# Performance work log

Measured on AMD Instinct MI355X. Metric: run time of the kernel, lower is better.

The kernel has to match this reference:

```python
import jax, jax.numpy as jnp
import numpy as np

N_NODES, N_EDGES = 100000, 1600000
F_IN, F_OUT = 256, 64
N_REL, N_BASES = 2, 30


def setup_inputs() -> dict:
    key = jax.random.key(0)
    ks = jax.random.split(key, 6)
    x = jax.random.normal(ks[0], (N_NODES, F_IN), jnp.float32)
    edge_index = jax.random.randint(ks[1], (2, N_EDGES), 0, N_NODES, jnp.int32)
    edge_type = jax.random.randint(ks[2], (N_EDGES,), 0, N_REL, jnp.int32)
    basis = jax.random.normal(ks[3], (N_BASES, F_IN, F_OUT), jnp.float32) * 0.05
    att = jax.random.normal(ks[4], (N_REL, N_BASES), jnp.float32) * 0.2
    root = jax.random.normal(ks[5], (F_IN, F_OUT), jnp.float32) * 0.05
    bias = jnp.zeros((F_OUT,), jnp.float32)
    return dict(x=x, edge_index=edge_index, edge_type=edge_type,
                basis=basis, att=att, root=root, bias=bias)


def reference(x, edge_index, edge_type, basis, att, root, bias):
    # RGCN with basis decomposition (PyG RGCNConv, aggr='mean', edge_norm=None)
    n = x.shape[0]
    # relation weights from bases: [R, F_in, F_out]
    w = jnp.einsum('rb,bio->rio', att, basis)
    # transform all nodes under every relation once (R is tiny): [R, N, F_out]
    h = jnp.einsum('ni,rio->rno', x, w)
    src, dst = edge_index[0], edge_index[1]
    # per-edge message x_src @ W[edge_type]: gather [E, F_out]
    msg = h[edge_type, src]
    # mean aggregation over incoming edges at each target node
    agg = jax.ops.segment_sum(msg, dst, num_segments=n)
    cnt = jax.ops.segment_sum(jnp.ones((msg.shape[0],), x.dtype), dst, num_segments=n)
    agg = agg / jnp.maximum(cnt, 1.0)[:, None]
    # update: self-loop (root) transform + bias
    return agg + x @ root + bias
```

## Files before the change

### kernel.cpp

```cpp
#include <hip/hip_runtime.h>
#include <hip/hip_bf16.h>

#define N_NODES 100000
#define N_EDGES 1600000
#define F_IN    256
#define F_OUT   64
#define N_REL   2
#define N_BASES 30
#define SCAN_BS 512
#define N_SBLK  ((N_NODES + SCAN_BS - 1) / SCAN_BS)
#define N_NT    12
#define N_KS    8

typedef __attribute__((ext_vector_type(8))) short bf16x8;
typedef __attribute__((ext_vector_type(4))) float f32x4;

__device__ inline unsigned short f2bf(float f) {
    unsigned u = __float_as_uint(f);
    unsigned r = u + 0x7FFF + ((u >> 16) & 1);
    return (unsigned short)(r >> 16);
}
__device__ inline float bf2f(unsigned short b) {
    return __uint_as_float(((unsigned)b) << 16);
}

__global__ __launch_bounds__(256) void wcomp_kernel(
    const float* __restrict__ att, const float* __restrict__ basis,
    const float* __restrict__ root,
    unsigned short* __restrict__ wb_hi, unsigned short* __restrict__ wb_lo)
{
    int idx = blockIdx.x * 256 + threadIdx.x;
    if (idx >= N_KS * N_NT * 64) return;
    const int lane  = idx & 63;
    const int nt    = (idx >> 6) % N_NT;
    const int ks    = idx / (N_NT * 64);
    const int c     = nt * 16 + (lane & 15);
    const int kbase = ks * 32 + (lane >> 4) * 8;
    const int m     = c >> 6;
    const int f     = c & 63;

    bf16x8 hi, lo;
    #pragma unroll
    for (int i = 0; i < 8; ++i) {
        int k = kbase + i;
        float v;
        if (m == 2) {
            v = root[k * F_OUT + f];
        } else {
            v = 0.f;
            #pragma unroll
            for (int b = 0; b < N_BASES; ++b)
                v += att[m * N_BASES + b] * basis[((long)b * F_IN + k) * F_OUT + f];
        }
        unsigned short h = f2bf(v);
        unsigned short l = f2bf(v - bf2f(h));
        hi[i] = (short)h;
        lo[i] = (short)l;
    }
    *reinterpret_cast<bf16x8*>(wb_hi + (long)idx * 8) = hi;
    *reinterpret_cast<bf16x8*>(wb_lo + (long)idx * 8) = lo;
}

__global__ __launch_bounds__(256) void gemm_kernel(
    const float* __restrict__ x,
    const unsigned short* __restrict__ wb_hi,
    const unsigned short* __restrict__ wb_lo,
    const float* __restrict__ bias,
    float* __restrict__ h, float* __restrict__ out)
{
    const int lane = threadIdx.x & 63;
    const int wv   = threadIdx.x >> 6;
    const long row0 = (long)blockIdx.x * 128 + wv * 32;
    if (row0 >= N_NODES) return;

    const int mrow = lane & 15;
    const int kgrp = lane >> 4;

    f32x4 acc[2][N_NT];
    #pragma unroll
    for (int mt = 0; mt < 2; ++mt)
        #pragma unroll
        for (int nt = 0; nt < N_NT; ++nt)
            acc[mt][nt] = (f32x4){0.f, 0.f, 0.f, 0.f};

    const float* xp = x + (row0 + mrow) * F_IN + kgrp * 8;

    for (int ks = 0; ks < N_KS; ++ks) {
        bf16x8 ah[2], al[2];
        #pragma unroll
        for (int mt = 0; mt < 2; ++mt) {
            const float* p = xp + (long)mt * 16 * F_IN + ks * 32;
            float4 f0 = *reinterpret_cast<const float4*>(p);
            float4 f1 = *reinterpret_cast<const float4*>(p + 4);
            float fv[8] = {f0.x, f0.y, f0.z, f0.w, f1.x, f1.y, f1.z, f1.w};
            #pragma unroll
            for (int i = 0; i < 8; ++i) {
                unsigned short hb = f2bf(fv[i]);
                ah[mt][i] = (short)hb;
                al[mt][i] = (short)f2bf(fv[i] - bf2f(hb));
            }
        }
        const unsigned short* bh_base = wb_hi + ((long)(ks * N_NT) * 64 + lane) * 8;
        const unsigned short* bl_base = wb_lo + ((long)(ks * N_NT) * 64 + lane) * 8;
        #pragma unroll
        for (int nt = 0; nt < N_NT; ++nt) {
            bf16x8 bh = *reinterpret_cast<const bf16x8*>(bh_base + (long)nt * 64 * 8);
            bf16x8 bl = *reinterpret_cast<const bf16x8*>(bl_base + (long)nt * 64 * 8);
            #pragma unroll
            for (int mt = 0; mt < 2; ++mt) {
                acc[mt][nt] = __builtin_amdgcn_mfma_f32_16x16x32_bf16(ah[mt], bh, acc[mt][nt], 0, 0, 0);
                acc[mt][nt] = __builtin_amdgcn_mfma_f32_16x16x32_bf16(al[mt], bh, acc[mt][nt], 0, 0, 0);
                acc[mt][nt] = __builtin_amdgcn_mfma_f32_16x16x32_bf16(ah[mt], bl, acc[mt][nt], 0, 0, 0);
            }
        }
    }

    const int ccol = lane & 15;
    const int rsub = (lane >> 4) * 4;
    #pragma unroll
    for (int mt = 0; mt < 2; ++mt) {
        #pragma unroll
        for (int nt = 0; nt < N_NT; ++nt) {
            const int rel = nt >> 2;
            const int fc  = (nt & 3) * 16 + ccol;
            float badd = (rel == 2) ? bias[fc] : 0.f;
            #pragma unroll
            for (int i = 0; i < 4; ++i) {
                long row = row0 + mt * 16 + rsub + i;
                float v = acc[mt][nt][i] + badd;
                if (rel == 2) out[row * F_OUT + fc] = v;
                else          h[((long)rel * N_NODES + row) * F_OUT + fc] = v;
            }
        }
    }
}

__global__ __launch_bounds__(256) void hist_kernel(
    const int* __restrict__ edge_index, int* __restrict__ hist)
{
    int e = blockIdx.x * 256 + threadIdx.x;
    if (e >= N_EDGES) return;
    atomicAdd(&hist[edge_index[N_EDGES + e]], 1);
}

__global__ __launch_bounds__(SCAN_BS) void scanA_kernel(
    const int* __restrict__ hist, int* __restrict__ offs, int* __restrict__ bsum)
{
    __shared__ int s[SCAN_BS];
    const int t = threadIdx.x;
    const int i = blockIdx.x * SCAN_BS + t;
    int v = (i < N_NODES) ? hist[i] : 0;
    s[t] = v;
    __syncthreads();
    #pragma unroll
    for (int off = 1; off < SCAN_BS; off <<= 1) {
        int y = (t >= off) ? s[t - off] : 0;
        __syncthreads();
        if (t >= off) s[t] += y;
        __syncthreads();
    }
    if (i < N_NODES) offs[i] = s[t] - v;
    if (t == SCAN_BS - 1) bsum[blockIdx.x] = s[t];
}

__global__ __launch_bounds__(256) void scanB_kernel(
    const int* __restrict__ bsum, int* __restrict__ bpre)
{
    __shared__ int s[256];
    const int t = threadIdx.x;
    int v = (t < N_SBLK) ? bsum[t] : 0;
    s[t] = v;
    __syncthreads();
    #pragma unroll
    for (int off = 1; off < 256; off <<= 1) {
        int y = (t >= off) ? s[t - off] : 0;
        __syncthreads();
        if (t >= off) s[t] += y;
        __syncthreads();
    }
    if (t < N_SBLK) bpre[t] = s[t] - v;
}

__global__ __launch_bounds__(256) void pass2_kernel(
    const int* __restrict__ edge_index, const int* __restrict__ edge_type,
    const int* __restrict__ offs, const int* __restrict__ bpre,
    int* __restrict__ cur, int* __restrict__ elist)
{
    int e = blockIdx.x * 256 + threadIdx.x;
    if (e >= N_EDGES) return;
    int src = edge_index[e];
    int dst = edge_index[N_EDGES + e];
    int et  = edge_type[e];
    int pos = offs[dst] + bpre[dst >> 9] + atomicAdd(&cur[dst], 1);
    elist[pos] = src | (et << 20);
}

__global__ __launch_bounds__(256) void gather_kernel(
    const int* __restrict__ hist, const int* __restrict__ offs,
    const int* __restrict__ bpre, const int* __restrict__ elist,
    const float* __restrict__ h, float* __restrict__ out)
{
    const int lane = threadIdx.x & 63;
    const int nid  = blockIdx.x * 4 + (threadIdx.x >> 6);
    if (nid >= N_NODES) return;
    const int cnt  = hist[nid];
    const int base = offs[nid] + bpre[nid >> 9];

    float acc = 0.f;
    int j = 0;
    for (; j + 4 <= cnt; j += 4) {
        int e0 = elist[base + j];
        int e1 = elist[base + j + 1];
        int e2 = elist[base + j + 2];
        int e3 = elist[base + j + 3];
        float v0 = h[((long)(e0 >> 20) * N_NODES + (e0 & 0xFFFFF)) * F_OUT + lane];
        float v1 = h[((long)(e1 >> 20) * N_NODES + (e1 & 0xFFFFF)) * F_OUT + lane];
        float v2 = h[((long)(e2 >> 20) * N_NODES + (e2 & 0xFFFFF)) * F_OUT + lane];
        float v3 = h[((long)(e3 >> 20) * N_NODES + (e3 & 0xFFFFF)) * F_OUT + lane];
        acc += v0; acc += v1; acc += v2; acc += v3;
    }
    for (; j < cnt; ++j) {
        int e = elist[base + j];
        acc += h[((long)(e >> 20) * N_NODES + (e & 0xFFFFF)) * F_OUT + lane];
    }
    float inv = 1.0f / fmaxf((float)cnt, 1.0f);
    out[(long)nid * F_OUT + lane] += acc * inv;
}

extern "C" void kernel_launch(void* const* d_in, const int* in_sizes, int n_in,
                              void* d_out, int out_size, void* d_ws, size_t ws_size,
                              hipStream_t stream)
{
    const float* x          = (const float*)d_in[0];
    const int*   edge_index = (const int*)  d_in[1];
    const int*   edge_type  = (const int*)  d_in[2];
    const float* basis      = (const float*)d_in[3];
    const float* att        = (const float*)d_in[4];
    const float* root       = (const float*)d_in[5];
    const float* bias       = (const float*)d_in[6];
    float* out = (float*)d_out;

    char* ws = (char*)d_ws;
    size_t off = 0;
    unsigned short* wb_hi = (unsigned short*)(ws + off); off += (size_t)N_KS * N_NT * 64 * 8 * 2;
    unsigned short* wb_lo = (unsigned short*)(ws + off); off += (size_t)N_KS * N_NT * 64 * 8 * 2;
    float* h     = (float*)(ws + off); off += (size_t)N_REL * N_NODES * F_OUT * 4;
    int*   hist  = (int*)  (ws + off); off += (size_t)N_NODES * 4;
    int*   cur   = (int*)  (ws + off); off += (size_t)N_NODES * 4;
    int*   offs  = (int*)  (ws + off); off += (size_t)N_NODES * 4;
    int*   bsum  = (int*)  (ws + off); off += (size_t)N_SBLK * 4;
    int*   bpre  = (int*)  (ws + off); off += (size_t)N_SBLK * 4;
    int*   elist = (int*)  (ws + off); off += (size_t)N_EDGES * 4;

    hipMemsetAsync(hist, 0, (size_t)2 * N_NODES * 4, stream);

    wcomp_kernel<<<(N_KS * N_NT * 64 + 255) / 256, 256, 0, stream>>>(
        att, basis, root, wb_hi, wb_lo);

    gemm_kernel<<<(N_NODES + 127) / 128, 256, 0, stream>>>(
        x, wb_hi, wb_lo, bias, h, out);

    hist_kernel<<<(N_EDGES + 255) / 256, 256, 0, stream>>>(edge_index, hist);

    scanA_kernel<<<N_SBLK, SCAN_BS, 0, stream>>>(hist, offs, bsum);

    scanB_kernel<<<1, 256, 0, stream>>>(bsum, bpre);

    pass2_kernel<<<(N_EDGES + 255) / 256, 256, 0, stream>>>(
        edge_index, edge_type, offs, bpre, cur, elist);

    gather_kernel<<<(N_NODES + 3) / 4, 256, 0, stream>>>(
        hist, offs, bpre, elist, h, out);
}
```

Baseline: 466.7 us.

## Replace per-node atomic CSR scatter with two-level bucket scatter plus local sort

Edges are first scattered into 128-node buckets using padded per-bucket atomic counters. A second kernel then places each bucket's edges into per-node CSR order using shared-memory atomics. This replaces 1.6M global atomics spread over 100K random counters, and the scattered writes that go with them, with fewer contended counters and more localized writes. The cost is an extra pass over the edge list and two extra launches. The gather loop is also unrolled to 8 edges so more loads are in flight at once.

```diff
diff --git a/kernel.cpp b/kernel.cpp
--- a/kernel.cpp
+++ b/kernel.cpp
@@ -11,6 +11,7 @@
 #define N_SBLK  ((N_NODES + SCAN_BS - 1) / SCAN_BS)
 #define N_NT    12
 #define N_KS    8
+#define NB      ((N_NODES + 127) / 128)
 
 typedef __attribute__((ext_vector_type(8))) short bf16x8;
 typedef __attribute__((ext_vector_type(4))) float f32x4;
@@ -181,18 +182,55 @@
     if (t < N_SBLK) bpre[t] = s[t] - v;
 }
 
-__global__ __launch_bounds__(256) void pass2_kernel(
+__global__ __launch_bounds__(256) void bbase_kernel(
+    const int* __restrict__ offs, const int* __restrict__ bpre,
+    int* __restrict__ bucket_base)
+{
+    int b = blockIdx.x * 256 + threadIdx.x;
+    if (b > NB) return;
+    int node = b << 7;
+    bucket_base[b] = (node < N_NODES) ? (offs[node] + bpre[node >> 9]) : N_EDGES;
+}
+
+__global__ __launch_bounds__(256) void binscatter_kernel(
     const int* __restrict__ edge_index, const int* __restrict__ edge_type,
-    const int* __restrict__ offs, const int* __restrict__ bpre,
-    int* __restrict__ cur, int* __restrict__ elist)
+    const int* __restrict__ bucket_base, int* __restrict__ bucket_cur,
+    int* __restrict__ belist)
 {
     int e = blockIdx.x * 256 + threadIdx.x;
     if (e >= N_EDGES) return;
     int src = edge_index[e];
     int dst = edge_index[N_EDGES + e];
     int et  = edge_type[e];
-    int pos = offs[dst] + bpre[dst >> 9] + atomicAdd(&cur[dst], 1);
-    elist[pos] = src | (et << 20);
+    int b   = dst >> 7;
+    int pos = bucket_base[b] + atomicAdd(&bucket_cur[b * 16], 1);
+    belist[pos] = src | (et << 17) | ((dst & 127) << 18);
+}
+
+__global__ __launch_bounds__(256) void sortlocal_kernel(
+    const int* __restrict__ bucket_base, const int* __restrict__ offs,
+    const int* __restrict__ bpre, const int* __restrict__ belist,
+    int* __restrict__ elist)
+{
+    __shared__ int cnt[128];
+    __shared__ int sbase[128];
+    const int b = blockIdx.x;
+    const int t = threadIdx.x;
+    const int node0 = b << 7;
+    if (t < 128) {
+        cnt[t] = 0;
+        int node = node0 + t;
+        sbase[t] = (node < N_NODES) ? (offs[node] + bpre[node >> 9]) : 0;
+    }
+    __syncthreads();
+    const int base = bucket_base[b];
+    const int next = bucket_base[b + 1];
+    for (int i = base + t; i < next; i += 256) {
+        int v = belist[i];
+        int dstlo = (v >> 18) & 127;
+        int pos = sbase[dstlo] + atomicAdd(&cnt[dstlo], 1);
+        elist[pos] = (v & 0x1FFFF) | (((v >> 17) & 1) << 20);
+    }
 }
 
 __global__ __launch_bounds__(256) void gather_kernel(
@@ -208,16 +246,25 @@
 
     float acc = 0.f;
     int j = 0;
+    for (; j + 8 <= cnt; j += 8) {
+        float v[8];
+        #pragma unroll
+        for (int q = 0; q < 8; ++q) {
+            int e = elist[base + j + q];
+            v[q] = h[((long)(e >> 20) * N_NODES + (e & 0xFFFFF)) * F_OUT + lane];
+        }
+        #pragma unroll
+        for (int q = 0; q < 8; ++q) acc += v[q];
+    }
     for (; j + 4 <= cnt; j += 4) {
-        int e0 = elist[base + j];
-        int e1 = elist[base + j + 1];
-        int e2 = elist[base + j + 2];
-        int e3 = elist[base + j + 3];
-        float v0 = h[((long)(e0 >> 20) * N_NODES + (e0 & 0xFFFFF)) * F_OUT + lane];
-        float v1 = h[((long)(e1 >> 20) * N_NODES + (e1 & 0xFFFFF)) * F_OUT + lane];
-        float v2 = h[((long)(e2 >> 20) * N_NODES + (e2 & 0xFFFFF)) * F_OUT + lane];
-        float v3 = h[((long)(e3 >> 20) * N_NODES + (e3 & 0xFFFFF)) * F_OUT + lane];
-        acc += v0; acc += v1; acc += v2; acc += v3;
+        float v[4];
+        #pragma unroll
+        for (int q = 0; q < 4; ++q) {
+            int e = elist[base + j + q];
+            v[q] = h[((long)(e >> 20) * N_NODES + (e & 0xFFFFF)) * F_OUT + lane];
+        }
+        #pragma unroll
+        for (int q = 0; q < 4; ++q) acc += v[q];
     }
     for (; j < cnt; ++j) {
         int e = elist[base + j];
@@ -244,15 +291,17 @@
     size_t off = 0;
     unsigned short* wb_hi = (unsigned short*)(ws + off); off += (size_t)N_KS * N_NT * 64 * 8 * 2;
     unsigned short* wb_lo = (unsigned short*)(ws + off); off += (size_t)N_KS * N_NT * 64 * 8 * 2;
-    float* h     = (float*)(ws + off); off += (size_t)N_REL * N_NODES * F_OUT * 4;
-    int*   hist  = (int*)  (ws + off); off += (size_t)N_NODES * 4;
-    int*   cur   = (int*)  (ws + off); off += (size_t)N_NODES * 4;
-    int*   offs  = (int*)  (ws + off); off += (size_t)N_NODES * 4;
-    int*   bsum  = (int*)  (ws + off); off += (size_t)N_SBLK * 4;
-    int*   bpre  = (int*)  (ws + off); off += (size_t)N_SBLK * 4;
-    int*   elist = (int*)  (ws + off); off += (size_t)N_EDGES * 4;
-
-    hipMemsetAsync(hist, 0, (size_t)2 * N_NODES * 4, stream);
+    float* h          = (float*)(ws + off); off += (size_t)N_REL * N_NODES * F_OUT * 4;
+    int*   hist       = (int*)  (ws + off); off += (size_t)N_NODES * 4;
+    int*   bucket_cur = (int*)  (ws + off); off += (size_t)NB * 16 * 4;
+    int*   offs       = (int*)  (ws + off); off += (size_t)N_NODES * 4;
+    int*   bsum       = (int*)  (ws + off); off += (size_t)N_SBLK * 4;
+    int*   bpre       = (int*)  (ws + off); off += (size_t)N_SBLK * 4;
+    int*   bucket_base= (int*)  (ws + off); off += (size_t)(NB + 1) * 4;
+    int*   belist     = (int*)  (ws + off); off += (size_t)N_EDGES * 4;
+    int*   elist      = (int*)  (ws + off); off += (size_t)N_EDGES * 4;
+
+    hipMemsetAsync(hist, 0, (size_t)(N_NODES + NB * 16) * 4, stream);
 
     wcomp_kernel<<<(N_KS * N_NT * 64 + 255) / 256, 256, 0, stream>>>(
         att, basis, root, wb_hi, wb_lo);
@@ -266,8 +315,13 @@
 
     scanB_kernel<<<1, 256, 0, stream>>>(bsum, bpre);
 
-    pass2_kernel<<<(N_EDGES + 255) / 256, 256, 0, stream>>>(
-        edge_index, edge_type, offs, bpre, cur, elist);
+    bbase_kernel<<<(NB + 256) / 256, 256, 0, stream>>>(offs, bpre, bucket_base);
+
+    binscatter_kernel<<<(N_EDGES + 255) / 256, 256, 0, stream>>>(
+        edge_index, edge_type, bucket_base, bucket_cur, belist);
+
+    sortlocal_kernel<<<NB, 256, 0, stream>>>(
+        bucket_base, offs, bpre, belist, elist);
 
     gather_kernel<<<(N_NODES + 3) / 4, 256, 0, stream>>>(
         hist, offs, bpre, elist, h, out);
```

After: 470.2 us. About the same (+0.7%).

## Replace per-node CSR build with 128-node bucket binning and LDS atomic aggregation

Applied to the files above, without the earlier changes.

The per-node histogram, two-level scan and CSR scatter are replaced by a coarser binning of edges into 128-destination buckets, split into 8 sub-cells by block index so scatter atomics contend less. The gather kernel now handles one bucket per block and accumulates messages into a shared-memory tile with LDS float atomics before writing the mean. This removes the per-node offset scan and per-node atomic cursor, and it makes the scan a single-block scan over roughly 6K cells. In exchange it adds LDS atomic contention, and the packed encoding gives the source index only 17 bits, which fits just under 131072 nodes. The scan is now serial in one block, and the summation order inside each bucket is nondeterministic.

```diff
diff --git a/kernel.cpp b/kernel.cpp
--- a/kernel.cpp
+++ b/kernel.cpp
@@ -7,10 +7,10 @@
 #define F_OUT   64
 #define N_REL   2
 #define N_BASES 30
-#define SCAN_BS 512
-#define N_SBLK  ((N_NODES + SCAN_BS - 1) / SCAN_BS)
 #define N_NT    12
 #define N_KS    8
+#define NB      ((N_NODES + 127) / 128)
+#define NCELL   (NB * 8)
 
 typedef __attribute__((ext_vector_type(8))) short bf16x8;
 typedef __attribute__((ext_vector_type(4))) float f32x4;
@@ -135,96 +135,97 @@
     }
 }
 
-__global__ __launch_bounds__(256) void hist_kernel(
-    const int* __restrict__ edge_index, int* __restrict__ hist)
+__global__ __launch_bounds__(256) void hist2_kernel(
+    const int* __restrict__ edge_index, int* __restrict__ hist,
+    int* __restrict__ h2)
 {
     int e = blockIdx.x * 256 + threadIdx.x;
     if (e >= N_EDGES) return;
-    atomicAdd(&hist[edge_index[N_EDGES + e]], 1);
-}
-
-__global__ __launch_bounds__(SCAN_BS) void scanA_kernel(
-    const int* __restrict__ hist, int* __restrict__ offs, int* __restrict__ bsum)
-{
-    __shared__ int s[SCAN_BS];
+    int dst = edge_index[N_EDGES + e];
+    atomicAdd(&hist[dst], 1);
+    atomicAdd(&h2[(dst >> 7) * 8 + (blockIdx.x & 7)], 1);
+}
+
+__global__ __launch_bounds__(1024) void bscan_kernel(
+    const int* __restrict__ h2, int* __restrict__ sub_base)
+{
+    __shared__ int s[1024];
+    __shared__ int carry;
     const int t = threadIdx.x;
-    const int i = blockIdx.x * SCAN_BS + t;
-    int v = (i < N_NODES) ? hist[i] : 0;
-    s[t] = v;
+    if (t == 0) carry = 0;
     __syncthreads();
-    #pragma unroll
-    for (int off = 1; off < SCAN_BS; off <<= 1) {
-        int y = (t >= off) ? s[t - off] : 0;
+    for (int base = 0; base < NCELL; base += 1024) {
+        int i = base + t;
+        int v = (i < NCELL) ? h2[i] : 0;
+        s[t] = v;
         __syncthreads();
-        if (t >= off) s[t] += y;
+        #pragma unroll
+        for (int off = 1; off < 1024; off <<= 1) {
+            int y = (t >= off) ? s[t - off] : 0;
+            __syncthreads();
+            s[t] += y;
+            __syncthreads();
+        }
+        int c = carry;
         __syncthreads();
-    }
-    if (i < N_NODES) offs[i] = s[t] - v;
-    if (t == SCAN_BS - 1) bsum[blockIdx.x] = s[t];
-}
-
-__global__ __launch_bounds__(256) void scanB_kernel(
-    const int* __restrict__ bsum, int* __restrict__ bpre)
-{
-    __shared__ int s[256];
-    const int t = threadIdx.x;
-    int v = (t < N_SBLK) ? bsum[t] : 0;
-    s[t] = v;
-    __syncthreads();
-    #pragma unroll
-    for (int off = 1; off < 256; off <<= 1) {
-        int y = (t >= off) ? s[t - off] : 0;
+        if (i < NCELL) sub_base[i] = c + s[t] - v;
+        if (t == 1023) carry = c + s[1023];
         __syncthreads();
-        if (t >= off) s[t] += y;
-        __syncthreads();
-    }
-    if (t < N_SBLK) bpre[t] = s[t] - v;
-}
-
-__global__ __launch_bounds__(256) void pass2_kernel(
+    }
+    if (t == 0) sub_base[NCELL] = carry;
+}
+
+__global__ __launch_bounds__(256) void binscatter_kernel(
     const int* __restrict__ edge_index, const int* __restrict__ edge_type,
-    const int* __restrict__ offs, const int* __restrict__ bpre,
-    int* __restrict__ cur, int* __restrict__ elist)
+    const int* __restrict__ sub_base, int* __restrict__ cur2,
+    int* __restrict__ belist)
 {
     int e = blockIdx.x * 256 + threadIdx.x;
     if (e >= N_EDGES) return;
     int src = edge_index[e];
     int dst = edge_index[N_EDGES + e];
     int et  = edge_type[e];
-    int pos = offs[dst] + bpre[dst >> 9] + atomicAdd(&cur[dst], 1);
-    elist[pos] = src | (et << 20);
-}
-
-__global__ __launch_bounds__(256) void gather_kernel(
-    const int* __restrict__ hist, const int* __restrict__ offs,
-    const int* __restrict__ bpre, const int* __restrict__ elist,
-    const float* __restrict__ h, float* __restrict__ out)
-{
-    const int lane = threadIdx.x & 63;
-    const int nid  = blockIdx.x * 4 + (threadIdx.x >> 6);
-    if (nid >= N_NODES) return;
-    const int cnt  = hist[nid];
-    const int base = offs[nid] + bpre[nid >> 9];
-
-    float acc = 0.f;
-    int j = 0;
-    for (; j + 4 <= cnt; j += 4) {
-        int e0 = elist[base + j];
-        int e1 = elist[base + j + 1];
-        int e2 = elist[base + j + 2];
-        int e3 = elist[base + j + 3];
-        float v0 = h[((long)(e0 >> 20) * N_NODES + (e0 & 0xFFFFF)) * F_OUT + lane];
-        float v1 = h[((long)(e1 >> 20) * N_NODES + (e1 & 0xFFFFF)) * F_OUT + lane];
-        float v2 = h[((long)(e2 >> 20) * N_NODES + (e2 & 0xFFFFF)) * F_OUT + lane];
-        float v3 = h[((long)(e3 >> 20) * N_NODES + (e3 & 0xFFFFF)) * F_OUT + lane];
-        acc += v0; acc += v1; acc += v2; acc += v3;
-    }
-    for (; j < cnt; ++j) {
-        int e = elist[base + j];
-        acc += h[((long)(e >> 20) * N_NODES + (e & 0xFFFFF)) * F_OUT + lane];
-    }
-    float inv = 1.0f / fmaxf((float)cnt, 1.0f);
-    out[(long)nid * F_OUT + lane] += acc * inv;
+    int cell = (dst >> 7) * 8 + (blockIdx.x & 7);
+    int pos = sub_base[cell] + atomicAdd(&cur2[cell * 16], 1);
+    belist[pos] = src | (et << 17) | ((dst & 127) << 18);
+}
+
+__global__ __launch_bounds__(512) void bucketgather_kernel(
+    const int* __restrict__ sub_base, const int* __restrict__ belist,
+    const int* __restrict__ hist, const float* __restrict__ h,
+    float* __restrict__ out)
+{
+    __shared__ float acc[128][64];
+    const int t    = threadIdx.x;
+    const int lane = t & 63;
+    const int wv   = t >> 6;
+    const int b    = blockIdx.x;
+
+    float* af = &acc[0][0];
+    #pragma unroll
+    for (int i = t; i < 128 * 64; i += 512) af[i] = 0.f;
+    __syncthreads();
+
+    const int beg = sub_base[b * 8];
+    const int end = sub_base[b * 8 + 8];
+    for (int i = beg + wv; i < end; i += 8) {
+        int v   = belist[i];
+        int src = v & 0x1FFFF;
+        int et  = (v >> 17) & 1;
+        int dlo = (v >> 18) & 127;
+        float val = h[((long)et * N_NODES + src) * F_OUT + lane];
+        atomicAdd(&acc[dlo][lane], val);
+    }
+    __syncthreads();
+
+    const int node0 = b << 7;
+    for (int r = wv; r < 128; r += 8) {
+        int node = node0 + r;
+        if (node < N_NODES) {
+            float inv = 1.0f / fmaxf((float)hist[node], 1.0f);
+            out[(long)node * F_OUT + lane] += acc[r][lane] * inv;
+        }
+    }
 }
 
 extern "C" void kernel_launch(void* const* d_in, const int* in_sizes, int n_in,
@@ -244,15 +245,14 @@
     size_t off = 0;
     unsigned short* wb_hi = (unsigned short*)(ws + off); off += (size_t)N_KS * N_NT * 64 * 8 * 2;
     unsigned short* wb_lo = (unsigned short*)(ws + off); off += (size_t)N_KS * N_NT * 64 * 8 * 2;
-    float* h     = (float*)(ws + off); off += (size_t)N_REL * N_NODES * F_OUT * 4;
-    int*   hist  = (int*)  (ws + off); off += (size_t)N_NODES * 4;
-    int*   cur   = (int*)  (ws + off); off += (size_t)N_NODES * 4;
-    int*   offs  = (int*)  (ws + off); off += (size_t)N_NODES * 4;
-    int*   bsum  = (int*)  (ws + off); off += (size_t)N_SBLK * 4;
-    int*   bpre  = (int*)  (ws + off); off += (size_t)N_SBLK * 4;
-    int*   elist = (int*)  (ws + off); off += (size_t)N_EDGES * 4;
-
-    hipMemsetAsync(hist, 0, (size_t)2 * N_NODES * 4, stream);
+    float* h        = (float*)(ws + off); off += (size_t)N_REL * N_NODES * F_OUT * 4;
+    int*   hist     = (int*)  (ws + off); off += (size_t)N_NODES * 4;
+    int*   h2       = (int*)  (ws + off); off += (size_t)NCELL * 4;
+    int*   cur2     = (int*)  (ws + off); off += (size_t)NCELL * 16 * 4;
+    int*   sub_base = (int*)  (ws + off); off += (size_t)(NCELL + 1) * 4;
+    int*   belist   = (int*)  (ws + off); off += (size_t)N_EDGES * 4;
+
+    hipMemsetAsync(hist, 0, (size_t)(N_NODES + NCELL + NCELL * 16) * 4, stream);
 
     wcomp_kernel<<<(N_KS * N_NT * 64 + 255) / 256, 256, 0, stream>>>(
         att, basis, root, wb_hi, wb_lo);
@@ -260,15 +260,14 @@
     gemm_kernel<<<(N_NODES + 127) / 128, 256, 0, stream>>>(
         x, wb_hi, wb_lo, bias, h, out);
 
-    hist_kernel<<<(N_EDGES + 255) / 256, 256, 0, stream>>>(edge_index, hist);
-
-    scanA_kernel<<<N_SBLK, SCAN_BS, 0, stream>>>(hist, offs, bsum);
-
-    scanB_kernel<<<1, 256, 0, stream>>>(bsum, bpre);
-
-    pass2_kernel<<<(N_EDGES + 255) / 256, 256, 0, stream>>>(
-        edge_index, edge_type, offs, bpre, cur, elist);
-
-    gather_kernel<<<(N_NODES + 3) / 4, 256, 0, stream>>>(
-        hist, offs, bpre, elist, h, out);
-}
+    hist2_kernel<<<(N_EDGES + 255) / 256, 256, 0, stream>>>(
+        edge_index, hist, h2);
+
+    bscan_kernel<<<1, 1024, 0, stream>>>(h2, sub_base);
+
+    binscatter_kernel<<<(N_EDGES + 255) / 256, 256, 0, stream>>>(
+        edge_index, edge_type, sub_base, cur2, belist);
+
+    bucketgather_kernel<<<NB, 512, 0, stream>>>(
+        sub_base, belist, hist, h, out);
+}
```

Result: slower. 1.138 ms (+143.8%).
